# Kernel tuning notes

Hardware: AMD Instinct MI355X
Metric: run time of the kernel (lower is better)

Reference implementation:

```python
import jax, jax.numpy as jnp
import numpy as np

FEATURE_IN = 4096
FEATURE_OUT = 4096
R = 16
ALPHA = 32.0


def setup_inputs() -> dict:
    key = jax.random.key(0)
    k_x, k_w, k_b, k_a = jax.random.split(key, 4)
    x = jax.random.normal(k_x, (4, 2048, FEATURE_IN), dtype=jnp.float32)
    # base linear (torch nn.Linear): weight [out, in], bias [out]
    bound = 1.0 / np.sqrt(FEATURE_IN)
    w = jax.random.uniform(k_w, (FEATURE_OUT, FEATURE_IN), dtype=jnp.float32, minval=-bound, maxval=bound)
    b = jax.random.uniform(k_b, (FEATURE_OUT,), dtype=jnp.float32, minval=-bound, maxval=bound)
    # lora_a: kaiming uniform over [feature_in, r]; lora_b: zeros -> use small randn so grads are nontrivial? No: faithful init is zeros, but zeros makes LoRA path trivially zero. Use kaiming for a, small random for b to exercise the math.
    gain = np.sqrt(2.0 / (1.0 + 5.0 ** 2))  # kaiming_uniform default a=sqrt(5)
    bound_a = gain * np.sqrt(3.0 / FEATURE_IN)
    lora_a = jax.random.uniform(k_a, (FEATURE_IN, R), dtype=jnp.float32, minval=-bound_a, maxval=bound_a)
    lora_b = jax.random.normal(jax.random.fold_in(key, 7), (R, FEATURE_OUT), dtype=jnp.float32) * 0.01
    return {"x": x, "w": w, "b": b, "lora_a": lora_a, "lora_b": lora_b}


def reference(x, w, b, lora_a, lora_b):
    # base linear: x @ W^T + b
    output1 = jnp.einsum('bsi,oi->bso', x, w) + b
    # faithful to source: materialize (A @ B) [feature_in, feature_out] first,
    # then x @ (A@B), scaled by alpha/r
    ab = jnp.matmul(lora_a, lora_b)  # [feature_in, feature_out]
    output2 = jnp.matmul(x, ab) * (ALPHA / R)
    return output2 + output1
```

## Files before the change

### kernel.cpp

```cpp
#include <hip/hip_runtime.h>
#include <cstdint>
#include <cstddef>

#define FEATURE_IN 4096
#define FEATURE_OUT 4096
#define RNK 16

typedef __bf16 bf16x8_t __attribute__((ext_vector_type(8)));
typedef __bf16 bf16x4_t __attribute__((ext_vector_type(4)));
typedef float f32x4_t __attribute__((ext_vector_type(4)));

#define FW_KB 128
#define FW_NB 32
#define NFUSE 4096
#define NCVTB 2048
#define CVT_THREADS (NCVTB * 256)
#define CVT_CHUNKS 16

__global__ __launch_bounds__(256) void prep_all(const float* __restrict__ x,
                                                uint16_t* __restrict__ xb,
                                                const float* __restrict__ w,
                                                const float* __restrict__ la,
                                                const float* __restrict__ lb,
                                                uint16_t* __restrict__ wf) {
    __shared__ float las[FW_KB * RNK];
    __shared__ float lbs[RNK * FW_NB];

    const int tid = threadIdx.x;

    if (blockIdx.x >= NFUSE) {
        const int tg = (blockIdx.x - NFUSE) * 256 + tid;
        const float4* xp = (const float4*)x;
        bf16x4_t* op = (bf16x4_t*)xb;
#pragma unroll
        for (int i = 0; i < CVT_CHUNKS; ++i) {
            const int idx = i * CVT_THREADS + tg;
            float4 v = xp[idx];
            bf16x4_t o;
            o[0] = (__bf16)v.x; o[1] = (__bf16)v.y; o[2] = (__bf16)v.z; o[3] = (__bf16)v.w;
            op[idx] = o;
        }
        return;
    }

    const int bid = blockIdx.x;
    const int kb = (bid & 31) * FW_KB;
    const int nb = (bid >> 5) * FW_NB;

    {
        const float4* src = (const float4*)(la + (size_t)kb * RNK);
        float4* dst = (float4*)las;
        dst[tid] = src[tid];
        dst[tid + 256] = src[tid + 256];
    }
#pragma unroll
    for (int f = tid; f < RNK * FW_NB; f += 256) {
        int r = f >> 5;
        int nl = f & 31;
        lbs[r * FW_NB + nl] = lb[(size_t)r * FEATURE_OUT + nb + nl];
    }
    __syncthreads();

    const int nl = tid >> 3;
    const int kq = tid & 7;

    f32x4_t bcol[4];
#pragma unroll
    for (int r4 = 0; r4 < 4; ++r4) {
        f32x4_t v;
#pragma unroll
        for (int j = 0; j < 4; ++j) v[j] = lbs[(r4 * 4 + j) * FW_NB + nl];
        bcol[r4] = v;
    }

    const f32x4_t* las4 = (const f32x4_t*)las;
    const float* wrow = w + (size_t)(nb + nl) * FEATURE_IN + kb + kq * 16;
    uint16_t* wfrow = wf + (size_t)(nb + nl) * FEATURE_IN + kb + kq * 16;

#pragma unroll
    for (int h = 0; h < 2; ++h) {
        float4 wv0 = ((const float4*)wrow)[h * 2 + 0];
        float4 wv1 = ((const float4*)wrow)[h * 2 + 1];
        float wfv[8] = {wv0.x, wv0.y, wv0.z, wv0.w, wv1.x, wv1.y, wv1.z, wv1.w};
        bf16x8_t o;
#pragma unroll
        for (int j = 0; j < 8; ++j) {
            const int k = kq * 16 + h * 8 + j;
            float s = 0.f;
#pragma unroll
            for (int rr = 0; rr < 4; ++rr) {
                const int r4 = (rr + kq) & 3;
                f32x4_t av = las4[k * 4 + r4];
                f32x4_t bv = bcol[r4];
                s += av[0] * bv[0] + av[1] * bv[1] + av[2] * bv[2] + av[3] * bv[3];
            }
            o[j] = (__bf16)(wfv[j] + 2.f * s);
        }
        ((bf16x8_t*)wfrow)[h] = o;
    }
}

#define BM 256
#define BN 256
#define BK 32
#define NT (FEATURE_IN / BK)

#define ABUF(b) ((b) * 32768)
#define BBUF(b) ((b) * 32768 + 16384)

#define READ_A0(b) do { _Pragma("unroll")                                                \
    for (int _mi = 0; _mi < 4; ++_mi)                                                    \
        af[_mi] = *(const bf16x8_t*)(lds + ABUF(b) + aoff[_mi]); } while (0)

#define READ_A1(b) do { _Pragma("unroll")                                                \
    for (int _mi = 0; _mi < 4; ++_mi)                                                    \
        af[_mi] = *(const bf16x8_t*)(lds + ABUF(b) + aoff[4 + _mi]); } while (0)

#define READ_B4(b) do { _Pragma("unroll")                                                \
    for (int _ni = 0; _ni < 4; ++_ni)                                                    \
        bq[_ni] = *(const bf16x8_t*)(lds + BBUF(b) + boff[_ni]); } while (0)

#define MFMA16(G) do { _Pragma("unroll")                                                 \
    for (int _mi = 0; _mi < 4; ++_mi) { _Pragma("unroll")                                \
        for (int _ni = 0; _ni < 4; ++_ni)                                                \
            acc[(G) * 4 + _mi][_ni] = __builtin_amdgcn_mfma_f32_16x16x32_bf16(           \
                af[_mi], bq[_ni], acc[(G) * 4 + _mi][_ni], 0, 0, 0); } } while (0)

#define GLL(SRC, DSTOFF)                                                                 \
    __builtin_amdgcn_global_load_lds(                                                    \
        (const __attribute__((address_space(1))) void*)(SRC),                            \
        (__attribute__((address_space(3))) void*)(lds + (DSTOFF) + wv * 1024), 16, 0, 0)

#define STAGE_A(b) do { GLL(pA0, ABUF(b)); GLL(pA1, ABUF(b) + 8192); } while (0)
#define STAGE_B(b) do { GLL(pB0, BBUF(b)); GLL(pB1, BBUF(b) + 8192); } while (0)

#define PBAR() __builtin_amdgcn_s_barrier()
#define PRIO1 __builtin_amdgcn_s_setprio(1)
#define PRIO0 __builtin_amdgcn_s_setprio(0)
#define VMCNT(n) asm volatile("s_waitcnt vmcnt(" #n ")" ::: "memory")

#define TILE_BODY(CUR, NXT)                                                              \
    READ_A0(CUR); READ_B4(CUR);                                                          \
    STAGE_A(NXT);                                                                        \
    PBAR();                                                                              \
    PRIO1; MFMA16(0); PRIO0;                                                             \
    PBAR();                                                                              \
    READ_A1(CUR);                                                                        \
    STAGE_B(NXT);                                                                        \
    PBAR();                                                                              \
    PRIO1; MFMA16(1); PRIO0;                                                             \
    VMCNT(8);                                                                            \
    PBAR();                                                                              \
    pA0 += BK; pA1 += BK; pB0 += BK; pB1 += BK;

#define DRAIN_BODY(CUR, NWAIT)                                                           \
    READ_A0(CUR); READ_B4(CUR);                                                          \
    PRIO1; MFMA16(0); PRIO0;                                                             \
    READ_A1(CUR);                                                                        \
    PRIO1; MFMA16(1); PRIO0;                                                             \
    VMCNT(NWAIT);                                                                        \
    PBAR();

__global__ __launch_bounds__(512, 2) void gemm256(const uint16_t* __restrict__ Au,
                                                  const uint16_t* __restrict__ Bu,
                                                  const float* __restrict__ bias,
                                                  float* __restrict__ C,
                                                  int M, int N, int K) {
    __shared__ __align__(16) char lds[131072];

    const __bf16* A = (const __bf16*)Au;
    const __bf16* B = (const __bf16*)Bu;

    const int tid  = threadIdx.x;
    const int wv   = tid >> 6;
    const int lane = tid & 63;
    const int waveM = wv >> 2;
    const int waveN = wv & 3;
    const int l15 = lane & 15;
    const int q   = lane >> 4;

    const int nbx = N / BN;
    const int nwg = nbx * (M / BM);
    const int bidlin = blockIdx.y * nbx + blockIdx.x;
    const int swz = (bidlin & 7) * (nwg >> 3) + (bidlin >> 3);
    const int by = swz / nbx;
    const int bx = swz - by * nbx;
    const int m0 = by * BM;
    const int n0 = bx * BN;

    const int srow = tid >> 2;
    const int sq   = ((tid & 3) - (srow >> 1)) & 3;
    const __bf16* pA0 = A + (size_t)(m0 + srow) * K + sq * 8;
    const __bf16* pA1 = pA0 + (size_t)128 * K;
    const __bf16* pB0 = B + (size_t)(n0 + srow) * K + sq * 8;
    const __bf16* pB1 = pB0 + (size_t)128 * K;

    int aoff[8], boff[4];
#pragma unroll
    for (int mi = 0; mi < 8; ++mi) {
        int row = waveM * 128 + mi * 16 + l15;
        aoff[mi] = row * 64 + (((row >> 1) + q) & 3) * 16;
    }
#pragma unroll
    for (int ni = 0; ni < 4; ++ni) {
        int row = waveN * 64 + ni * 16 + l15;
        boff[ni] = row * 64 + (((row >> 1) + q) & 3) * 16;
    }

    f32x4_t acc[8][4];
#pragma unroll
    for (int mi = 0; mi < 8; ++mi)
#pragma unroll
        for (int ni = 0; ni < 4; ++ni)
            acc[mi][ni] = (f32x4_t)0.f;

    bf16x8_t af[4], bq[4];

    STAGE_A(0); STAGE_B(0); pA0 += BK; pA1 += BK; pB0 += BK; pB1 += BK;
    STAGE_A(1); STAGE_B(1); pA0 += BK; pA1 += BK; pB0 += BK; pB1 += BK;
    STAGE_A(2); STAGE_B(2); pA0 += BK; pA1 += BK; pB0 += BK; pB1 += BK;
    VMCNT(8);
    PBAR();

#pragma unroll 1
    for (int i = 0; i < 31; ++i) {
        TILE_BODY(0, 3)
        TILE_BODY(1, 0)
        TILE_BODY(2, 1)
        TILE_BODY(3, 2)
    }
    TILE_BODY(0, 3)

    DRAIN_BODY(1, 4)
    DRAIN_BODY(2, 0)
    READ_A0(3); READ_B4(3);
    PRIO1; MFMA16(0); PRIO0;
    READ_A1(3);
    PRIO1; MFMA16(1); PRIO0;

#pragma unroll
    for (int ni = 0; ni < 4; ++ni) {
        const int col = n0 + waveN * 64 + ni * 16 + l15;
        const float bv = bias[col];
#pragma unroll
        for (int mi = 0; mi < 8; ++mi) {
            const int row = m0 + waveM * 128 + mi * 16 + q * 4;
            float* op = C + (size_t)row * N + col;
#pragma unroll
            for (int j = 0; j < 4; ++j)
                op[(size_t)j * N] = acc[mi][ni][j] + bv;
        }
    }
}

extern "C" void kernel_launch(void* const* d_in, const int* in_sizes, int n_in,
                              void* d_out, int out_size, void* d_ws, size_t ws_size,
                              hipStream_t stream) {
    const float* x  = (const float*)d_in[0];
    const float* w  = (const float*)d_in[1];
    const float* b  = (const float*)d_in[2];
    const float* la = (const float*)d_in[3];
    const float* lb = (const float*)d_in[4];
    float* out = (float*)d_out;

    const int M = in_sizes[0] / FEATURE_IN;
    const int K = FEATURE_IN;
    const int N = FEATURE_OUT;

    uint16_t* xb = (uint16_t*)d_ws;
    uint16_t* wf = (uint16_t*)((char*)d_ws + (size_t)M * K * 2);

    prep_all<<<NFUSE + NCVTB, 256, 0, stream>>>(x, xb, w, la, lb, wf);

    {
        dim3 grid(N / BN, M / BM);
        gemm256<<<grid, 512, 0, stream>>>(xb, wf, b, out, M, N, K);
    }
}
```

Before: 513.6 us.

## Software-pipeline LDS fragment reads across tiles with double-buffered registers

Restructures the main GEMM loop so the A/B fragments for the next K-tile are read from LDS while the second half of the current tile's MFMAs runs, using double-buffered register fragments. Barriers per tile drop from four to two, and sched_barrier pins the ordering of reads and MFMAs. The aim is to hide LDS read latency behind matrix math. The cost is higher register pressure under launch_bounds(512,2) and tighter vmcnt/barrier correctness requirements.

After: 509.0 us. About the same (-0.9%).

```diff
diff --git a/kernel.cpp b/kernel.cpp
--- a/kernel.cpp
+++ b/kernel.cpp
@@ -108,23 +108,28 @@
 #define ABUF(b) ((b) * 32768)
 #define BBUF(b) ((b) * 32768 + 16384)
 
-#define READ_A0(b) do { _Pragma("unroll")                                                \
-    for (int _mi = 0; _mi < 4; ++_mi)                                                    \
-        af[_mi] = *(const bf16x8_t*)(lds + ABUF(b) + aoff[_mi]); } while (0)
-
-#define READ_A1(b) do { _Pragma("unroll")                                                \
-    for (int _mi = 0; _mi < 4; ++_mi)                                                    \
-        af[_mi] = *(const bf16x8_t*)(lds + ABUF(b) + aoff[4 + _mi]); } while (0)
-
-#define READ_B4(b) do { _Pragma("unroll")                                                \
-    for (int _ni = 0; _ni < 4; ++_ni)                                                    \
-        bq[_ni] = *(const bf16x8_t*)(lds + BBUF(b) + boff[_ni]); } while (0)
-
-#define MFMA16(G) do { _Pragma("unroll")                                                 \
+#define MFMA16X(S) do { _Pragma("unroll")                                                \
     for (int _mi = 0; _mi < 4; ++_mi) { _Pragma("unroll")                                \
         for (int _ni = 0; _ni < 4; ++_ni)                                                \
-            acc[(G) * 4 + _mi][_ni] = __builtin_amdgcn_mfma_f32_16x16x32_bf16(           \
-                af[_mi], bq[_ni], acc[(G) * 4 + _mi][_ni], 0, 0, 0); } } while (0)
+            acc[_mi][_ni] = __builtin_amdgcn_mfma_f32_16x16x32_bf16(                     \
+                afx[S][_mi], bqr[S][_ni], acc[_mi][_ni], 0, 0, 0); } } while (0)
+
+#define MFMA16Y(S) do { _Pragma("unroll")                                                \
+    for (int _mi = 0; _mi < 4; ++_mi) { _Pragma("unroll")                                \
+        for (int _ni = 0; _ni < 4; ++_ni)                                                \
+            acc[4 + _mi][_ni] = __builtin_amdgcn_mfma_f32_16x16x32_bf16(                 \
+                afy[_mi], bqr[S][_ni], acc[4 + _mi][_ni], 0, 0, 0); } } while (0)
+
+#define READ_AFY(b) do { _Pragma("unroll")                                               \
+    for (int _mi = 0; _mi < 4; ++_mi)                                                    \
+        afy[_mi] = *(const bf16x8_t*)(lds + ABUF(b) + aoff[4 + _mi]); } while (0)
+
+#define READ_R0(b, SN) do { _Pragma("unroll")                                            \
+    for (int _mi = 0; _mi < 4; ++_mi)                                                    \
+        afx[SN][_mi] = *(const bf16x8_t*)(lds + ABUF(b) + aoff[_mi]);                    \
+    _Pragma("unroll")                                                                    \
+    for (int _ni = 0; _ni < 4; ++_ni)                                                    \
+        bqr[SN][_ni] = *(const bf16x8_t*)(lds + BBUF(b) + boff[_ni]); } while (0)
 
 #define GLL(SRC, DSTOFF)                                                                 \
     __builtin_amdgcn_global_load_lds(                                                    \
@@ -138,27 +143,31 @@
 #define PRIO1 __builtin_amdgcn_s_setprio(1)
 #define PRIO0 __builtin_amdgcn_s_setprio(0)
 #define VMCNT(n) asm volatile("s_waitcnt vmcnt(" #n ")" ::: "memory")
-
-#define TILE_BODY(CUR, NXT)                                                              \
-    READ_A0(CUR); READ_B4(CUR);                                                          \
+#define SCHEDB() __builtin_amdgcn_sched_barrier(0)
+
+#define TILE_BODY(CUR, NXT, S, SN)                                                       \
+    READ_AFY(CUR);                                                                       \
     STAGE_A(NXT);                                                                        \
+    SCHEDB();                                                                            \
+    PRIO1; MFMA16X(S); PRIO0;                                                            \
+    VMCNT(6);                                                                            \
     PBAR();                                                                              \
-    PRIO1; MFMA16(0); PRIO0;                                                             \
-    PBAR();                                                                              \
-    READ_A1(CUR);                                                                        \
+    READ_R0((CUR + 1) & 3, SN);                                                          \
     STAGE_B(NXT);                                                                        \
-    PBAR();                                                                              \
-    PRIO1; MFMA16(1); PRIO0;                                                             \
-    VMCNT(8);                                                                            \
+    SCHEDB();                                                                            \
+    PRIO1; MFMA16Y(S); PRIO0;                                                            \
     PBAR();                                                                              \
     pA0 += BK; pA1 += BK; pB0 += BK; pB1 += BK;
 
-#define DRAIN_BODY(CUR, NWAIT)                                                           \
-    READ_A0(CUR); READ_B4(CUR);                                                          \
-    PRIO1; MFMA16(0); PRIO0;                                                             \
-    READ_A1(CUR);                                                                        \
-    PRIO1; MFMA16(1); PRIO0;                                                             \
+#define TAIL_BODY(CUR, S, SN, NWAIT)                                                     \
+    READ_AFY(CUR);                                                                       \
+    SCHEDB();                                                                            \
+    PRIO1; MFMA16X(S); PRIO0;                                                            \
     VMCNT(NWAIT);                                                                        \
+    PBAR();                                                                              \
+    READ_R0((CUR + 1) & 3, SN);                                                          \
+    SCHEDB();                                                                            \
+    PRIO1; MFMA16Y(S); PRIO0;                                                            \
     PBAR();
 
 __global__ __launch_bounds__(512, 2) void gemm256(const uint16_t* __restrict__ Au,
@@ -214,29 +223,30 @@
         for (int ni = 0; ni < 4; ++ni)
             acc[mi][ni] = (f32x4_t)0.f;
 
-    bf16x8_t af[4], bq[4];
+    bf16x8_t afx[2][4], afy[4], bqr[2][4];
 
     STAGE_A(0); STAGE_B(0); pA0 += BK; pA1 += BK; pB0 += BK; pB1 += BK;
     STAGE_A(1); STAGE_B(1); pA0 += BK; pA1 += BK; pB0 += BK; pB1 += BK;
     STAGE_A(2); STAGE_B(2); pA0 += BK; pA1 += BK; pB0 += BK; pB1 += BK;
     VMCNT(8);
     PBAR();
+    READ_R0(0, 0);
 
 #pragma unroll 1
     for (int i = 0; i < 31; ++i) {
-        TILE_BODY(0, 3)
-        TILE_BODY(1, 0)
-        TILE_BODY(2, 1)
-        TILE_BODY(3, 2)
-    }
-    TILE_BODY(0, 3)
-
-    DRAIN_BODY(1, 4)
-    DRAIN_BODY(2, 0)
-    READ_A0(3); READ_B4(3);
-    PRIO1; MFMA16(0); PRIO0;
-    READ_A1(3);
-    PRIO1; MFMA16(1); PRIO0;
+        TILE_BODY(0, 3, 0, 1)
+        TILE_BODY(1, 0, 1, 0)
+        TILE_BODY(2, 1, 0, 1)
+        TILE_BODY(3, 2, 1, 0)
+    }
+    TILE_BODY(0, 3, 0, 1)
+
+    TAIL_BODY(1, 1, 0, 4)
+    TAIL_BODY(2, 0, 1, 0)
+    READ_AFY(3);
+    SCHEDB();
+    PRIO1; MFMA16X(1); PRIO0;
+    PRIO1; MFMA16Y(1); PRIO0;
 
 #pragma unroll
     for (int ni = 0; ni < 4; ++ni) {
```
